# Optimization experiments

Hardware: AMD Instinct MI355X
Metric: run time of the kernel (lower is better)

Reference implementation:

```python
import jax, jax.numpy as jnp
import numpy as np
from jax import lax

B, N, M = 4, 16384, 512
RADIUS2 = 4.0        # radius=2 (hard-coded in forward), compare squared distances
BALL_K = 64          # k=64 hard-coded in forward
KNN_K = 9            # opt.node_knn_k_1
SIGMA_LB = 0.001     # opt.loss_sigma_lower_bound

_DIMS = [("conv1", 6, 64), ("conv2", 64, 64), ("conv3", 64, 64),
         ("conv4", 128, 128), ("conv5", 128, 128),
         ("knnb1", 131, 256), ("knnb2", 256, 256), ("knnb3", 256, 256),
         ("knna1", 512, 512), ("knna2", 512, 512),
         ("mlp1", 640, 512), ("mlp2", 512, 256)]


def setup_inputs() -> dict:
    key = jax.random.key(0)
    ks = jax.random.split(key, 6)
    inp = {
        "x": jax.random.normal(ks[0], (B, 3, N), jnp.float32),
        "sn": jax.random.normal(ks[1], (B, 3, N), jnp.float32),
        "node": jax.random.normal(ks[2], (B, 3, M), jnp.float32),
    }
    for i, (name, cin, cout) in enumerate(_DIMS):
        k = jax.random.fold_in(ks[3], i)
        inp[name + "_w"] = jax.random.normal(k, (cout, cin), jnp.float32) * np.float32(1.0 / np.sqrt(cin))
        inp[name + "_b"] = jnp.zeros((cout,), jnp.float32)
    inp["mlp3_w"] = jax.random.normal(ks[4], (4, 256), jnp.float32) * np.float32(1e-4)  # .normal_(0, 0.0001)
    inp["mlp3_b"] = jnp.zeros((4,), jnp.float32)
    return inp


def _conv(f, w, b, act=True):
    # 1x1 conv over (B,C,M) or (B,C,M,K): channel matmul + bias (+relu)
    y = jnp.einsum('oc,bc...->bo...', w, f) + b.reshape((1, -1) + (1,) * (f.ndim - 2))
    return jax.nn.relu(y) if act else y


def _sqdist(a, b):
    # a: (B,3,Ma), b: (B,3,Nb) -> (B,Ma,Nb) squared euclidean distances
    aa = jnp.sum(a * a, axis=1)
    bb = jnp.sum(b * b, axis=1)
    ab = jnp.einsum('bcm,bcn->bmn', a, b)
    return aa[:, :, None] + bb[:, None, :] - 2.0 * ab


def _gather(feat, idx):
    # feat: (B,C,Nb), idx: (B,Mq,K) -> (B,C,Mq,K)
    Bq, C, _ = feat.shape
    _, Mq, K = idx.shape
    flat = jnp.broadcast_to(idx.reshape(Bq, 1, Mq * K), (Bq, C, Mq * K))
    return jnp.take_along_axis(feat, flat, axis=2).reshape(Bq, C, Mq, K)


def _ball_query(sqd, radius2, k):
    # first k point indices (in original order) with dist<radius, padded by the first hit
    n = sqd.shape[2]
    mask = sqd < radius2
    keyi = jnp.where(mask, jnp.arange(n, dtype=jnp.int32)[None, None, :], jnp.int32(n))
    _, idx = lax.top_k(-keyi, k)  # k smallest keys == first k in-ball indices
    count = jnp.sum(mask, axis=2, keepdims=True)
    return jnp.where(jnp.arange(k)[None, None, :] < count, idx, idx[:, :, :1])


def reference(x, sn, node,
              conv1_w, conv1_b, conv2_w, conv2_b, conv3_w, conv3_b,
              conv4_w, conv4_b, conv5_w, conv5_b,
              knnb1_w, knnb1_b, knnb2_w, knnb2_b, knnb3_w, knnb3_b,
              knna1_w, knna1_b, knna2_w, knna2_b,
              mlp1_w, mlp1_b, mlp2_w, mlp2_b, mlp3_w, mlp3_b):
    x_aug = jnp.concatenate([x, sn], axis=1)                      # (B,6,N)
    idx = _ball_query(_sqdist(node, x), RADIUS2, BALL_K)          # (B,M,64)
    xb = _gather(x_aug, idx)                                      # (B,6,M,64)
    xb = jnp.concatenate([xb[:, :3] - node[:, :, :, None], xb[:, 3:]], axis=1)
    f = _conv(_conv(_conv(xb, conv1_w, conv1_b), conv2_w, conv2_b), conv3_w, conv3_b)
    fmax = jnp.max(f, axis=3, keepdims=True)
    f = jnp.concatenate([f, jnp.broadcast_to(fmax, f.shape)], axis=1)
    f = _conv(_conv(f, conv4_w, conv4_b), conv5_w, conv5_b)
    feat1 = jnp.max(f, axis=3)                                    # (B,128,M)

    # GeneralKNNFusionModule: query=node, database=node, x=feat1, K=KNN_K
    _, knn_idx = lax.top_k(-_sqdist(node, node), KNN_K)           # (B,M,K) nearest nodes
    coords = _gather(node, knn_idx) - node[:, :, :, None]         # (B,3,M,K)
    g = jnp.concatenate([coords, _gather(feat1, knn_idx)], axis=1)  # (B,131,M,K)
    g = _conv(_conv(_conv(g, knnb1_w, knnb1_b), knnb2_w, knnb2_b), knnb3_w, knnb3_b)
    gmax = jnp.max(g, axis=3, keepdims=True)
    g = jnp.concatenate([g, jnp.broadcast_to(gmax, g.shape)], axis=1)
    g = _conv(_conv(g, knna1_w, knna1_b), knna2_w, knna2_b)
    feat2 = jnp.max(g, axis=3)                                    # (B,512,M)

    h = jnp.concatenate([feat1, feat2], axis=1)                   # (B,640,M)
    h = _conv(_conv(h, mlp1_w, mlp1_b), mlp2_w, mlp2_b)
    ksig = _conv(h, mlp3_w, mlp3_b, act=False)                    # (B,4,M)
    keypoints = ksig[:, :3] + node
    sigmas = jax.nn.softplus(ksig[:, 3]) + SIGMA_LB
    return node, keypoints, sigmas
```

## Files before the change

kernel.cpp:

```cpp
#include <hip/hip_runtime.h>

typedef unsigned short u16;
typedef unsigned int u32;
typedef __bf16 bf16x8 __attribute__((ext_vector_type(8)));
typedef float floatx4 __attribute__((ext_vector_type(4)));
typedef unsigned short u16x8 __attribute__((ext_vector_type(8)));
typedef unsigned int u32x4 __attribute__((ext_vector_type(4)));

static constexpr int B_ = 4;
static constexpr int N_ = 16384;
static constexpr int M_ = 512;

__device__ __forceinline__ u16 f2bf(float f) {
    u32 u = __float_as_uint(f);
    u32 r = (u + 0x7fffu + ((u >> 16) & 1u)) >> 16;
    return (u16)r;
}
__device__ __forceinline__ float bf2f(u16 x) {
    return __uint_as_float(((u32)x) << 16);
}
__device__ __forceinline__ u32 pack2(float a, float b) {
    return (u32)f2bf(a) | ((u32)f2bf(b) << 16);
}

__global__ void pack_x_kernel(const float* __restrict__ x, float4* __restrict__ pk) {
    int t = blockIdx.x * 256 + threadIdx.x;
    int b = t >> 14, n = t & (N_ - 1);
    const float* xb = x + (size_t)b * 3 * N_;
    float px = xb[n], py = xb[N_ + n], pz = xb[2 * N_ + n];
    pk[t] = make_float4(px, py, pz, px * px + py * py + pz * pz);
}

__global__ __launch_bounds__(256) void ball_query_kernel(
    const float4* __restrict__ pk, const float* __restrict__ node, int* __restrict__ idx) {
    int bm = blockIdx.x;
    int b = bm >> 9, m = bm & 511;
    int tid = threadIdx.x, wave = tid >> 6, lane = tid & 63;
    __shared__ int sidx[4][64];
    __shared__ int scnt[4];

    const float4* pb = pk + ((size_t)b << 14);
    float nx = node[((size_t)b * 3 + 0) * M_ + m];
    float ny = node[((size_t)b * 3 + 1) * M_ + m];
    float nz = node[((size_t)b * 3 + 2) * M_ + m];
    float aa = nx * nx + ny * ny + nz * nz;

    int cnt = 0;
    int base = wave * 4096;
    for (int n0 = base; n0 < base + 4096; n0 += 64) {
        float4 p = pb[n0 + lane];
        float d = aa + p.w - 2.0f * (nx * p.x + ny * p.y + nz * p.z);
        bool inb = d < 4.0f;
        unsigned long long mask = __ballot(inb);
        if (inb && cnt < 64) {
            int pos = cnt + __popcll(mask & ((1ull << lane) - 1ull));
            if (pos < 64) sidx[wave][pos] = n0 + lane;
        }
        cnt += __popcll(mask);
        if (cnt >= 64) break;
    }
    if (lane == 0) scnt[wave] = cnt;
    __syncthreads();
    if (tid < 64) {
        int total = scnt[0] + scnt[1] + scnt[2] + scnt[3];
        int v = 0;
        if (total > 0) {
            int lim = total < 64 ? total : 64;
            int slot = tid < lim ? tid : 0;
            int w = 0, pre = 0;
            while (w < 3 && slot >= pre + scnt[w]) { pre += scnt[w]; ++w; }
            v = sidx[w][slot - pre];
        }
        idx[(size_t)bm * 64 + tid] = v;
    }
}

__global__ void knn_kernel(const float* __restrict__ node, int* __restrict__ knn) {
    int bm = blockIdx.x;
    int b = bm >> 9, m = bm & 511;
    int lane = threadIdx.x;
    const float* nb = node + (size_t)b * 3 * M_;
    float nx = nb[m], ny = nb[M_ + m], nz = nb[2 * M_ + m];
    float aa = nx * nx + ny * ny + nz * nz;

    float dist[8];
    int didx[8];
#pragma unroll
    for (int i = 0; i < 8; ++i) {
        int n = lane + i * 64;
        float px = nb[n], py = nb[M_ + n], pz = nb[2 * M_ + n];
        float bb = px * px + py * py + pz * pz;
        float ab = nx * px + ny * py + nz * pz;
        dist[i] = aa + bb - 2.0f * ab;
        didx[i] = n;
    }
    for (int r = 0; r < 9; ++r) {
        float bv = dist[0]; int bi = didx[0]; int bslot = 0;
#pragma unroll
        for (int i = 1; i < 8; ++i) {
            if (dist[i] < bv || (dist[i] == bv && didx[i] < bi)) {
                bv = dist[i]; bi = didx[i]; bslot = i;
            }
        }
        float rv = bv; int ri = bi;
        for (int off = 32; off > 0; off >>= 1) {
            float ov = __shfl_down(rv, off);
            int   oi = __shfl_down(ri, off);
            if (ov < rv || (ov == rv && oi < ri)) { rv = ov; ri = oi; }
        }
        ri = __shfl(ri, 0);
        if (lane == 0) knn[(size_t)bm * 9 + r] = ri;
        if (bi == ri) dist[bslot] = 3.0e38f;
    }
}

struct WConvArgs { const float* src[12]; };

__global__ void convert_weights_kernel(WConvArgs args, u16* __restrict__ dst) {
    const int CI[12] = {6, 64, 64, 128, 128, 131, 256, 256, 512, 512, 640, 512};
    const int KP[12] = {32, 64, 64, 128, 128, 160, 256, 256, 512, 512, 640, 512};
    const int OFF[13] = {0, 2048, 6144, 10240, 26624, 43008, 83968, 149504,
                         215040, 477184, 739328, 1067008, 1198080};
    int e = blockIdx.x * 256 + threadIdx.x;
    if (e >= 1198080) return;
    int w = 0;
    while (e >= OFF[w + 1]) ++w;
    int local = e - OFF[w];
    int kp = KP[w];
    int co = local / kp, k = local - co * kp;
    float v = 0.0f;
    if (w == 5) {
        if (k < 3) v = args.src[5][(size_t)co * 131 + k];
        else if (k >= 8 && k < 136) v = args.src[5][(size_t)co * 131 + (k - 5)];
    } else if (k < CI[w]) {
        v = args.src[w][(size_t)co * CI[w] + k];
    }
    dst[e] = f2bf(v);
}

static constexpr int RS = 136;

__device__ __forceinline__ bf16x8 ldsA(const u16* act, int rf, int l15, int quad, int ks) {
    return *(const bf16x8*)(act + (rf * 16 + l15) * RS + ks * 32 + quad * 8);
}
__device__ __forceinline__ bf16x8 ldW(const u16* W, int ks, int l15, int quad, int kstride) {
    return *(const bf16x8*)(W + (size_t)l15 * kstride + ks * 32 + quad * 8);
}

__global__ __launch_bounds__(256) void fused_stage1_kernel(
    const float* __restrict__ x, const float* __restrict__ sn,
    const float* __restrict__ node, const int* __restrict__ idx,
    const u16* __restrict__ Wbf,
    const float* __restrict__ b1, const float* __restrict__ b2,
    const float* __restrict__ b3, const float* __restrict__ b4,
    const float* __restrict__ b5, u16* __restrict__ h) {
    __shared__ __align__(16) u16 act[64 * RS];
    __shared__ __align__(16) u16 mv[64];
    int bm = blockIdx.x;
    int b = bm >> 9, m = bm & 511;
    int tid = threadIdx.x, wave = tid >> 6, lane = tid & 63;
    int quad = lane >> 4, l15 = lane & 15;

    {
        int row = tid & 63, grp = tid >> 6;
        int j = idx[(size_t)bm * 64 + row];
        const float* xb = x + (size_t)b * 3 * N_;
        const float* sb = sn + (size_t)b * 3 * N_;
        if (grp == 0) {
            float c0 = xb[j]      - node[((size_t)b * 3 + 0) * M_ + m];
            float c1 = xb[N_ + j] - node[((size_t)b * 3 + 1) * M_ + m];
            *(u32*)(act + row * RS) = pack2(c0, c1);
        } else if (grp == 1) {
            float c2 = xb[2 * N_ + j] - node[((size_t)b * 3 + 2) * M_ + m];
            *(u32*)(act + row * RS + 2) = pack2(c2, sb[j]);
        } else if (grp == 2) {
            *(u32*)(act + row * RS + 4) = pack2(sb[N_ + j], sb[2 * N_ + j]);
        } else {
            *(u32*)(act + row * RS + 6) = 0u;
            u32x4* r = (u32x4*)(act + row * RS + 8);
            r[0] = (u32x4){0u, 0u, 0u, 0u};
            r[1] = (u32x4){0u, 0u, 0u, 0u};
            r[2] = (u32x4){0u, 0u, 0u, 0u};
        }
    }
    __syncthreads();

    {
        const u16* Wp = Wbf + 0 + (size_t)(wave * 16) * 32;
        bf16x8 bw = ldW(Wp, 0, l15, quad, 32);
        bf16x8 a[4];
#pragma unroll
        for (int rf = 0; rf < 4; ++rf) a[rf] = ldsA(act, rf, l15, quad, 0);
        floatx4 c[4];
#pragma unroll
        for (int rf = 0; rf < 4; ++rf)
            c[rf] = __builtin_amdgcn_mfma_f32_16x16x32_bf16(a[rf], bw, (floatx4){0.f,0.f,0.f,0.f}, 0, 0, 0);
        float bias = b1[wave * 16 + l15];
        __syncthreads();
#pragma unroll
        for (int rf = 0; rf < 4; ++rf)
#pragma unroll
            for (int r = 0; r < 4; ++r)
                act[(rf * 16 + quad * 4 + r) * RS + wave * 16 + l15] = f2bf(fmaxf(c[rf][r] + bias, 0.0f));
        __syncthreads();
    }

    const int WOFF23[2] = {2048, 6144};
    const float* bp23[2] = {b2, b3};
#pragma unroll 1
    for (int cv = 0; cv < 2; ++cv) {
        const u16* Wp = Wbf + WOFF23[cv] + (size_t)(wave * 16) * 64;
        bf16x8 bw[2], a[4][2];
#pragma unroll
        for (int ks = 0; ks < 2; ++ks) bw[ks] = ldW(Wp, ks, l15, quad, 64);
#pragma unroll
        for (int rf = 0; rf < 4; ++rf)
#pragma unroll
            for (int ks = 0; ks < 2; ++ks) a[rf][ks] = ldsA(act, rf, l15, quad, ks);
        floatx4 c[4] = {};
#pragma unroll
        for (int ks = 0; ks < 2; ++ks)
#pragma unroll
            for (int rf = 0; rf < 4; ++rf)
                c[rf] = __builtin_amdgcn_mfma_f32_16x16x32_bf16(a[rf][ks], bw[ks], c[rf], 0, 0, 0);
        float bias = bp23[cv][wave * 16 + l15];
        float v[4][4];
        float mx = 0.0f;
#pragma unroll
        for (int rf = 0; rf < 4; ++rf)
#pragma unroll
            for (int r = 0; r < 4; ++r) {
                v[rf][r] = fmaxf(c[rf][r] + bias, 0.0f);
                mx = fmaxf(mx, v[rf][r]);
            }
        __syncthreads();
#pragma unroll
        for (int rf = 0; rf < 4; ++rf)
#pragma unroll
            for (int r = 0; r < 4; ++r)
                act[(rf * 16 + quad * 4 + r) * RS + wave * 16 + l15] = f2bf(v[rf][r]);
        if (cv == 1) {
            mx = fmaxf(mx, __shfl_xor(mx, 16));
            mx = fmaxf(mx, __shfl_xor(mx, 32));
            if (quad == 0) mv[wave * 16 + l15] = f2bf(mx);
        }
        __syncthreads();
    }

    {
        const u16* Wp = Wbf + 10240 + (size_t)(wave * 32) * 128;
        bf16x8 bw[2][4];
#pragma unroll
        for (int cf = 0; cf < 2; ++cf)
#pragma unroll
            for (int ks = 0; ks < 4; ++ks)
                bw[cf][ks] = ldW(Wp + (size_t)cf * 16 * 128, ks, l15, quad, 128);
        bf16x8 a01[4][2];
#pragma unroll
        for (int rf = 0; rf < 4; ++rf)
#pragma unroll
            for (int ks = 0; ks < 2; ++ks) a01[rf][ks] = ldsA(act, rf, l15, quad, ks);
        bf16x8 am2 = *(const bf16x8*)(mv + quad * 8);
        bf16x8 am3 = *(const bf16x8*)(mv + 32 + quad * 8);
        floatx4 c[4][2] = {};
#pragma unroll
        for (int ks = 0; ks < 4; ++ks) {
#pragma unroll
            for (int rf = 0; rf < 4; ++rf) {
                bf16x8 a = (ks < 2) ? a01[rf][ks] : (ks == 2 ? am2 : am3);
#pragma unroll
                for (int cf = 0; cf < 2; ++cf)
                    c[rf][cf] = __builtin_amdgcn_mfma_f32_16x16x32_bf16(a, bw[cf][ks], c[rf][cf], 0, 0, 0);
            }
        }
        float bias[2];
#pragma unroll
        for (int cf = 0; cf < 2; ++cf) bias[cf] = b4[wave * 32 + cf * 16 + l15];
        __syncthreads();
#pragma unroll
        for (int rf = 0; rf < 4; ++rf)
#pragma unroll
            for (int cf = 0; cf < 2; ++cf)
#pragma unroll
                for (int r = 0; r < 4; ++r)
                    act[(rf * 16 + quad * 4 + r) * RS + wave * 32 + cf * 16 + l15] =
                        f2bf(fmaxf(c[rf][cf][r] + bias[cf], 0.0f));
        __syncthreads();
    }

    {
        const u16* Wp = Wbf + 26624 + (size_t)(wave * 32) * 128;
        bf16x8 bw[2][4];
#pragma unroll
        for (int cf = 0; cf < 2; ++cf)
#pragma unroll
            for (int ks = 0; ks < 4; ++ks)
                bw[cf][ks] = ldW(Wp + (size_t)cf * 16 * 128, ks, l15, quad, 128);
        floatx4 c[4][2] = {};
#pragma unroll
        for (int ks = 0; ks < 4; ++ks) {
#pragma unroll
            for (int rf = 0; rf < 4; ++rf) {
                bf16x8 a = ldsA(act, rf, l15, quad, ks);
#pragma unroll
                for (int cf = 0; cf < 2; ++cf)
                    c[rf][cf] = __builtin_amdgcn_mfma_f32_16x16x32_bf16(a, bw[cf][ks], c[rf][cf], 0, 0, 0);
            }
        }
#pragma unroll
        for (int cf = 0; cf < 2; ++cf) {
            float bias = b5[wave * 32 + cf * 16 + l15];
            float mx = 0.0f;
#pragma unroll
            for (int rf = 0; rf < 4; ++rf)
#pragma unroll
                for (int r = 0; r < 4; ++r)
                    mx = fmaxf(mx, fmaxf(c[rf][cf][r] + bias, 0.0f));
            mx = fmaxf(mx, __shfl_xor(mx, 16));
            mx = fmaxf(mx, __shfl_xor(mx, 32));
            if (quad == 0) h[(size_t)bm * 640 + wave * 32 + cf * 16 + l15] = f2bf(mx);
        }
    }
}

template <int KS, int CF, int RF, int RSx>
__device__ __forceinline__ void conv_inplace(u16* act, const u16* __restrict__ W0, int KP,
                                             const float* __restrict__ bias, int cb,
                                             int l15, int quad) {
    floatx4 acc[RF][CF];
#pragma unroll
    for (int rf = 0; rf < RF; ++rf)
#pragma unroll
        for (int cf = 0; cf < CF; ++cf) acc[rf][cf] = (floatx4){0.f, 0.f, 0.f, 0.f};

    bf16x8 bwA[CF], bwB[CF];
#pragma unroll
    for (int cf = 0; cf < CF; ++cf)
        bwA[cf] = *(const bf16x8*)(W0 + (size_t)(cb + cf * 16 + l15) * KP + quad * 8);

#pragma unroll
    for (int ks = 0; ks < KS; ++ks) {
        bf16x8* cur = (ks % 2 == 0) ? bwA : bwB;
        bf16x8* nxt = (ks % 2 == 0) ? bwB : bwA;
        if (ks + 1 < KS) {
#pragma unroll
            for (int cf = 0; cf < CF; ++cf)
                nxt[cf] = *(const bf16x8*)(W0 + (size_t)(cb + cf * 16 + l15) * KP +
                                           (ks + 1) * 32 + quad * 8);
        }
#pragma unroll
        for (int rf = 0; rf < RF; ++rf) {
            bf16x8 a = *(const bf16x8*)(act + (rf * 16 + l15) * RSx + ks * 32 + quad * 8);
#pragma unroll
            for (int cf = 0; cf < CF; ++cf)
                acc[rf][cf] = __builtin_amdgcn_mfma_f32_16x16x32_bf16(a, cur[cf], acc[rf][cf], 0, 0, 0);
        }
    }
    __syncthreads();
#pragma unroll
    for (int cf = 0; cf < CF; ++cf) {
        float bs = bias[cb + cf * 16 + l15];
#pragma unroll
        for (int rf = 0; rf < RF; ++rf)
#pragma unroll
            for (int r = 0; r < 4; ++r)
                act[(rf * 16 + quad * 4 + r) * RSx + cb + cf * 16 + l15] =
                    f2bf(fmaxf(acc[rf][cf][r] + bs, 0.0f));
    }
    __syncthreads();
}

static constexpr int RS2 = 520;

__global__ __launch_bounds__(512, 1) void fused_stage2_kernel(
    const float* __restrict__ node, u16* __restrict__ h, const int* __restrict__ knn,
    const u16* __restrict__ Wbf,
    const float* __restrict__ bb1, const float* __restrict__ bb2,
    const float* __restrict__ bb3, const float* __restrict__ ba1,
    const float* __restrict__ ba2) {
    __shared__ __align__(16) u16 act[80 * RS2];
    int blk = blockIdx.x;
    int node0 = blk * 8;
    int b = node0 >> 9;
    int tid = threadIdx.x, wave = tid >> 6, lane = tid & 63;
    int quad = lane >> 4, l15 = lane & 15;
    (void)lane;

    for (int e = tid; e < 80 * 20; e += 512)
        *(u16x8*)(act + (e / 20) * RS2 + (e % 20) * 8) = (u16x8){0,0,0,0,0,0,0,0};
    __syncthreads();
    for (int e = tid; e < 72 * 3; e += 512) {
        int r = e / 3, c = e - r * 3;
        int nodei = node0 + r / 9;
        int j = knn[(size_t)nodei * 9 + (r % 9)];
        float v = node[((size_t)b * 3 + c) * M_ + j] - node[((size_t)b * 3 + c) * M_ + (nodei & 511)];
        act[r * RS2 + c] = f2bf(v);
    }
    for (int e = tid; e < 72 * 16; e += 512) {
        int r = e >> 4, s = e & 15;
        int nodei = node0 + r / 9;
        int j = knn[(size_t)nodei * 9 + (r % 9)];
        *(u16x8*)(act + r * RS2 + 8 + s * 8) =
            *(const u16x8*)(h + (size_t)(b * 512 + j) * 640 + s * 8);
    }
    __syncthreads();

    conv_inplace<5, 2, 5, RS2>(act, Wbf + 43008, 160, bb1, wave * 32, l15, quad);
    conv_inplace<8, 2, 5, RS2>(act, Wbf + 83968, 256, bb2, wave * 32, l15, quad);
    conv_inplace<8, 2, 5, RS2>(act, Wbf + 149504, 256, bb3, wave * 32, l15, quad);

    for (int e = tid; e < 8 * 32; e += 512) {
        int li = e >> 5, s = e & 31;
        int r0 = li * 9;
        float mx[8];
#pragma unroll
        for (int i = 0; i < 8; ++i) mx[i] = -3.0e38f;
#pragma unroll
        for (int kk = 0; kk < 9; ++kk) {
            u16x8 v = *(const u16x8*)(act + (r0 + kk) * RS2 + s * 8);
#pragma unroll
            for (int i = 0; i < 8; ++i) mx[i] = fmaxf(mx[i], bf2f(v[i]));
        }
        u16x8 o;
#pragma unroll
        for (int i = 0; i < 8; ++i) o[i] = f2bf(mx[i]);
#pragma unroll
        for (int kk = 0; kk < 9; ++kk)
            *(u16x8*)(act + (r0 + kk) * RS2 + 256 + s * 8) = o;
    }
    __syncthreads();

    conv_inplace<16, 4, 5, RS2>(act, Wbf + 215040, 512, ba1, wave * 64, l15, quad);
    conv_inplace<16, 4, 5, RS2>(act, Wbf + 477184, 512, ba2, wave * 64, l15, quad);

    for (int e = tid; e < 8 * 64; e += 512) {
        int li = e >> 6, s = e & 63;
        int r0 = li * 9;
        float mx[8];
#pragma unroll
        for (int i = 0; i < 8; ++i) mx[i] = -3.0e38f;
#pragma unroll
        for (int kk = 0; kk < 9; ++kk) {
            u16x8 v = *(const u16x8*)(act + (r0 + kk) * RS2 + s * 8);
#pragma unroll
            for (int i = 0; i < 8; ++i) mx[i] = fmaxf(mx[i], bf2f(v[i]));
        }
        u16x8 o;
#pragma unroll
        for (int i = 0; i < 8; ++i) o[i] = f2bf(mx[i]);
        *(u16x8*)(h + (size_t)(node0 + li) * 640 + 128 + s * 8) = o;
    }
}

static constexpr int RS3 = 648;

__global__ __launch_bounds__(512, 1) void fused_stage3_kernel(
    const float* __restrict__ node, const u16* __restrict__ h,
    const u16* __restrict__ Wbf,
    const float* __restrict__ bm1, const float* __restrict__ bm2,
    const float* __restrict__ w3, const float* __restrict__ b3,
    float* __restrict__ out) {
    __shared__ __align__(16) u16 act[16 * RS3];
    int blk = blockIdx.x;
    int node0 = blk * 16;
    int tid = threadIdx.x, lane = tid & 63, wave = tid >> 6;
    int quad = lane >> 4, l15 = lane & 15;

    for (int e = tid; e < 16 * 80; e += 512) {
        int r = e / 80, seg = e - r * 80;
        *(u16x8*)(act + r * RS3 + seg * 8) = *(const u16x8*)(h + (size_t)(node0 + r) * 640 + seg * 8);
    }
    __syncthreads();

    conv_inplace<20, 4, 1, RS3>(act, Wbf + 739328, 640, bm1, wave * 64, l15, quad);
    conv_inplace<16, 2, 1, RS3>(act, Wbf + 1067008, 512, bm2, wave * 32, l15, quad);

    if (tid < 64) {
        int li = tid >> 2, oc = tid & 3;
        const u16* row = act + li * RS3;
        const float* wrow = w3 + oc * 256;
        float a = 0.0f;
        for (int c = 0; c < 256; c += 4) {
            a += bf2f(row[c]) * wrow[c];
            a += bf2f(row[c + 1]) * wrow[c + 1];
            a += bf2f(row[c + 2]) * wrow[c + 2];
            a += bf2f(row[c + 3]) * wrow[c + 3];
        }
        a += b3[oc];
        int nodei = node0 + li;
        int b = nodei >> 9, m = nodei & 511;
        if (oc < 3) {
            float nv = node[((size_t)b * 3 + oc) * M_ + m];
            out[((size_t)b * 3 + oc) * M_ + m] = nv;
            out[6144 + ((size_t)b * 3 + oc) * M_ + m] = nv + a;
        } else {
            out[12288 + nodei] = fmaxf(a, 0.0f) + log1pf(expf(-fabsf(a))) + 0.001f;
        }
    }
}

extern "C" void kernel_launch(void* const* d_in, const int* in_sizes, int n_in,
                              void* d_out, int out_size, void* d_ws, size_t ws_size,
                              hipStream_t stream) {
    (void)in_sizes; (void)n_in; (void)out_size; (void)ws_size;
    const float* x = (const float*)d_in[0];
    const float* sn = (const float*)d_in[1];
    const float* node = (const float*)d_in[2];
    const float* W[13];
    const float* Bs[13];
    for (int i = 0; i < 13; ++i) {
        W[i] = (const float*)d_in[3 + 2 * i];
        Bs[i] = (const float*)d_in[4 + 2 * i];
    }
    float* out = (float*)d_out;

    char* ws = (char*)d_ws;
    int* idx = (int*)(ws + 0);
    int* knn = (int*)(ws + 524288);
    u16* Wbf = (u16*)(ws + 598016);
    u16* h   = (u16*)(ws + 2994176);
    float4* pk = (float4*)(ws + 5615616);

    WConvArgs wa;
    for (int w = 0; w < 12; ++w) wa.src[w] = W[w];
    convert_weights_kernel<<<(1198080 + 255) / 256, 256, 0, stream>>>(wa, Wbf);

    pack_x_kernel<<<256, 256, 0, stream>>>(x, pk);
    ball_query_kernel<<<2048, 256, 0, stream>>>(pk, node, idx);
    knn_kernel<<<2048, 64, 0, stream>>>(node, knn);

    fused_stage1_kernel<<<2048, 256, 0, stream>>>(x, sn, node, idx, Wbf,
                                                  Bs[0], Bs[1], Bs[2], Bs[3], Bs[4], h);
    fused_stage2_kernel<<<256, 512, 0, stream>>>(node, h, knn, Wbf,
                                                 Bs[5], Bs[6], Bs[7], Bs[8], Bs[9]);
    fused_stage3_kernel<<<128, 512, 0, stream>>>(node, h, Wbf, Bs[10], Bs[11],
                                                 W[12], Bs[12], out);
}
```

Measured before the change: 262.1 us.

## Rebalance work split across fused stage kernels: two nodes per stage1 block, wider stage2, smaller stage3

Stage1 now processes two ball-query groups per block (128 rows), so each loaded weight fragment is reused across twice as many MFMA tiles and half as many blocks are launched. Stage2 doubles its block to 1024 threads, with each wave owning half as many output channels. Stage3 handles 8 nodes per block with zero-padded rows, doubling the grid to 256 blocks for better CU coverage at the cost of wasted MFMA work on padded rows. Higher register pressure in stage1 and the larger stage2 blocks may reduce occupancy.

```diff
diff --git a/kernel.cpp b/kernel.cpp
--- a/kernel.cpp
+++ b/kernel.cpp
@@ -147,58 +147,58 @@
     return *(const bf16x8*)(W + (size_t)l15 * kstride + ks * 32 + quad * 8);
 }
 
-__global__ __launch_bounds__(256) void fused_stage1_kernel(
+__global__ __launch_bounds__(256, 2) void fused_stage1_kernel(
     const float* __restrict__ x, const float* __restrict__ sn,
     const float* __restrict__ node, const int* __restrict__ idx,
     const u16* __restrict__ Wbf,
     const float* __restrict__ b1, const float* __restrict__ b2,
     const float* __restrict__ b3, const float* __restrict__ b4,
     const float* __restrict__ b5, u16* __restrict__ h) {
-    __shared__ __align__(16) u16 act[64 * RS];
-    __shared__ __align__(16) u16 mv[64];
-    int bm = blockIdx.x;
-    int b = bm >> 9, m = bm & 511;
+    __shared__ __align__(16) u16 act[128 * RS];
+    __shared__ __align__(16) u16 mv[2][64];
+    int blk = blockIdx.x;
+    int bm0 = blk * 2;
     int tid = threadIdx.x, wave = tid >> 6, lane = tid & 63;
     int quad = lane >> 4, l15 = lane & 15;
 
     {
-        int row = tid & 63, grp = tid >> 6;
-        int j = idx[(size_t)bm * 64 + row];
+        int row = tid & 127, grp = tid >> 7;
+        int bm = bm0 + (row >> 6);
+        int b = bm >> 9, m = bm & 511;
+        int j = idx[(size_t)bm * 64 + (row & 63)];
         const float* xb = x + (size_t)b * 3 * N_;
         const float* sb = sn + (size_t)b * 3 * N_;
+        u16* r = act + row * RS;
         if (grp == 0) {
-            float c0 = xb[j]      - node[((size_t)b * 3 + 0) * M_ + m];
-            float c1 = xb[N_ + j] - node[((size_t)b * 3 + 1) * M_ + m];
-            *(u32*)(act + row * RS) = pack2(c0, c1);
-        } else if (grp == 1) {
+            float c0 = xb[j]          - node[((size_t)b * 3 + 0) * M_ + m];
+            float c1 = xb[N_ + j]     - node[((size_t)b * 3 + 1) * M_ + m];
             float c2 = xb[2 * N_ + j] - node[((size_t)b * 3 + 2) * M_ + m];
-            *(u32*)(act + row * RS + 2) = pack2(c2, sb[j]);
-        } else if (grp == 2) {
-            *(u32*)(act + row * RS + 4) = pack2(sb[N_ + j], sb[2 * N_ + j]);
+            *(u32*)(r)     = pack2(c0, c1);
+            *(u32*)(r + 2) = pack2(c2, sb[j]);
         } else {
-            *(u32*)(act + row * RS + 6) = 0u;
-            u32x4* r = (u32x4*)(act + row * RS + 8);
-            r[0] = (u32x4){0u, 0u, 0u, 0u};
-            r[1] = (u32x4){0u, 0u, 0u, 0u};
-            r[2] = (u32x4){0u, 0u, 0u, 0u};
+            *(u32*)(r + 4) = pack2(sb[N_ + j], sb[2 * N_ + j]);
+            *(u32*)(r + 6) = 0u;
+            u32x4* z = (u32x4*)(r + 8);
+            z[0] = (u32x4){0u, 0u, 0u, 0u};
+            z[1] = (u32x4){0u, 0u, 0u, 0u};
+            z[2] = (u32x4){0u, 0u, 0u, 0u};
         }
     }
     __syncthreads();
 
     {
-        const u16* Wp = Wbf + 0 + (size_t)(wave * 16) * 32;
+        const u16* Wp = Wbf + (size_t)(wave * 16) * 32;
         bf16x8 bw = ldW(Wp, 0, l15, quad, 32);
-        bf16x8 a[4];
-#pragma unroll
-        for (int rf = 0; rf < 4; ++rf) a[rf] = ldsA(act, rf, l15, quad, 0);
-        floatx4 c[4];
-#pragma unroll
-        for (int rf = 0; rf < 4; ++rf)
-            c[rf] = __builtin_amdgcn_mfma_f32_16x16x32_bf16(a[rf], bw, (floatx4){0.f,0.f,0.f,0.f}, 0, 0, 0);
+        floatx4 c[8];
+#pragma unroll
+        for (int rf = 0; rf < 8; ++rf) {
+            bf16x8 a = ldsA(act, rf, l15, quad, 0);
+            c[rf] = __builtin_amdgcn_mfma_f32_16x16x32_bf16(a, bw, (floatx4){0.f,0.f,0.f,0.f}, 0, 0, 0);
+        }
         float bias = b1[wave * 16 + l15];
         __syncthreads();
 #pragma unroll
-        for (int rf = 0; rf < 4; ++rf)
+        for (int rf = 0; rf < 8; ++rf)
 #pragma unroll
             for (int r = 0; r < 4; ++r)
                 act[(rf * 16 + quad * 4 + r) * RS + wave * 16 + l15] = f2bf(fmaxf(c[rf][r] + bias, 0.0f));
@@ -210,39 +210,40 @@
 #pragma unroll 1
     for (int cv = 0; cv < 2; ++cv) {
         const u16* Wp = Wbf + WOFF23[cv] + (size_t)(wave * 16) * 64;
-        bf16x8 bw[2], a[4][2];
-#pragma unroll
-        for (int ks = 0; ks < 2; ++ks) bw[ks] = ldW(Wp, ks, l15, quad, 64);
-#pragma unroll
-        for (int rf = 0; rf < 4; ++rf)
-#pragma unroll
-            for (int ks = 0; ks < 2; ++ks) a[rf][ks] = ldsA(act, rf, l15, quad, ks);
-        floatx4 c[4] = {};
+        bf16x8 bw0 = ldW(Wp, 0, l15, quad, 64);
+        bf16x8 bw1 = ldW(Wp, 1, l15, quad, 64);
+        floatx4 c[8] = {};
 #pragma unroll
         for (int ks = 0; ks < 2; ++ks)
 #pragma unroll
-            for (int rf = 0; rf < 4; ++rf)
-                c[rf] = __builtin_amdgcn_mfma_f32_16x16x32_bf16(a[rf][ks], bw[ks], c[rf], 0, 0, 0);
+            for (int rf = 0; rf < 8; ++rf) {
+                bf16x8 a = ldsA(act, rf, l15, quad, ks);
+                c[rf] = __builtin_amdgcn_mfma_f32_16x16x32_bf16(a, ks ? bw1 : bw0, c[rf], 0, 0, 0);
+            }
         float bias = bp23[cv][wave * 16 + l15];
-        float v[4][4];
-        float mx = 0.0f;
-#pragma unroll
-        for (int rf = 0; rf < 4; ++rf)
+        float mxA = 0.0f, mxB = 0.0f;
+#pragma unroll
+        for (int rf = 0; rf < 8; ++rf)
 #pragma unroll
             for (int r = 0; r < 4; ++r) {
-                v[rf][r] = fmaxf(c[rf][r] + bias, 0.0f);
-                mx = fmaxf(mx, v[rf][r]);
+                float v = fmaxf(c[rf][r] + bias, 0.0f);
+                if (rf < 4) mxA = fmaxf(mxA, v); else mxB = fmaxf(mxB, v);
             }
         __syncthreads();
 #pragma unroll
-        for (int rf = 0; rf < 4; ++rf)
+        for (int rf = 0; rf < 8; ++rf)
 #pragma unroll
             for (int r = 0; r < 4; ++r)
-                act[(rf * 16 + quad * 4 + r) * RS + wave * 16 + l15] = f2bf(v[rf][r]);
+                act[(rf * 16 + quad * 4 + r) * RS + wave * 16 + l15] = f2bf(fmaxf(c[rf][r] + bias, 0.0f));
         if (cv == 1) {
-            mx = fmaxf(mx, __shfl_xor(mx, 16));
-            mx = fmaxf(mx, __shfl_xor(mx, 32));
-            if (quad == 0) mv[wave * 16 + l15] = f2bf(mx);
+            mxA = fmaxf(mxA, __shfl_xor(mxA, 16));
+            mxA = fmaxf(mxA, __shfl_xor(mxA, 32));
+            mxB = fmaxf(mxB, __shfl_xor(mxB, 16));
+            mxB = fmaxf(mxB, __shfl_xor(mxB, 32));
+            if (quad == 0) {
+                mv[0][wave * 16 + l15] = f2bf(mxA);
+                mv[1][wave * 16 + l15] = f2bf(mxB);
+            }
         }
         __syncthreads();
     }
@@ -255,30 +256,23 @@
 #pragma unroll
             for (int ks = 0; ks < 4; ++ks)
                 bw[cf][ks] = ldW(Wp + (size_t)cf * 16 * 128, ks, l15, quad, 128);
-        bf16x8 a01[4][2];
-#pragma unroll
-        for (int rf = 0; rf < 4; ++rf)
-#pragma unroll
-            for (int ks = 0; ks < 2; ++ks) a01[rf][ks] = ldsA(act, rf, l15, quad, ks);
-        bf16x8 am2 = *(const bf16x8*)(mv + quad * 8);
-        bf16x8 am3 = *(const bf16x8*)(mv + 32 + quad * 8);
-        floatx4 c[4][2] = {};
-#pragma unroll
-        for (int ks = 0; ks < 4; ++ks) {
-#pragma unroll
-            for (int rf = 0; rf < 4; ++rf) {
-                bf16x8 a = (ks < 2) ? a01[rf][ks] : (ks == 2 ? am2 : am3);
+        floatx4 c[8][2] = {};
+#pragma unroll
+        for (int ks = 0; ks < 4; ++ks)
+#pragma unroll
+            for (int rf = 0; rf < 8; ++rf) {
+                bf16x8 a = (ks < 2) ? ldsA(act, rf, l15, quad, ks)
+                                    : *(const bf16x8*)(&mv[rf >> 2][(ks - 2) * 32 + quad * 8]);
 #pragma unroll
                 for (int cf = 0; cf < 2; ++cf)
                     c[rf][cf] = __builtin_amdgcn_mfma_f32_16x16x32_bf16(a, bw[cf][ks], c[rf][cf], 0, 0, 0);
             }
-        }
         float bias[2];
 #pragma unroll
         for (int cf = 0; cf < 2; ++cf) bias[cf] = b4[wave * 32 + cf * 16 + l15];
         __syncthreads();
 #pragma unroll
-        for (int rf = 0; rf < 4; ++rf)
+        for (int rf = 0; rf < 8; ++rf)
 #pragma unroll
             for (int cf = 0; cf < 2; ++cf)
 #pragma unroll
@@ -296,29 +290,35 @@
 #pragma unroll
             for (int ks = 0; ks < 4; ++ks)
                 bw[cf][ks] = ldW(Wp + (size_t)cf * 16 * 128, ks, l15, quad, 128);
-        floatx4 c[4][2] = {};
-#pragma unroll
-        for (int ks = 0; ks < 4; ++ks) {
-#pragma unroll
-            for (int rf = 0; rf < 4; ++rf) {
+        floatx4 c[8][2] = {};
+#pragma unroll
+        for (int ks = 0; ks < 4; ++ks)
+#pragma unroll
+            for (int rf = 0; rf < 8; ++rf) {
                 bf16x8 a = ldsA(act, rf, l15, quad, ks);
 #pragma unroll
                 for (int cf = 0; cf < 2; ++cf)
                     c[rf][cf] = __builtin_amdgcn_mfma_f32_16x16x32_bf16(a, bw[cf][ks], c[rf][cf], 0, 0, 0);
             }
-        }
 #pragma unroll
         for (int cf = 0; cf < 2; ++cf) {
             float bias = b5[wave * 32 + cf * 16 + l15];
-            float mx = 0.0f;
-#pragma unroll
-            for (int rf = 0; rf < 4; ++rf)
-#pragma unroll
-                for (int r = 0; r < 4; ++r)
-                    mx = fmaxf(mx, fmaxf(c[rf][cf][r] + bias, 0.0f));
-            mx = fmaxf(mx, __shfl_xor(mx, 16));
-            mx = fmaxf(mx, __shfl_xor(mx, 32));
-            if (quad == 0) h[(size_t)bm * 640 + wave * 32 + cf * 16 + l15] = f2bf(mx);
+            float mxA = 0.0f, mxB = 0.0f;
+#pragma unroll
+            for (int rf = 0; rf < 8; ++rf)
+#pragma unroll
+                for (int r = 0; r < 4; ++r) {
+                    float v = fmaxf(c[rf][cf][r] + bias, 0.0f);
+                    if (rf < 4) mxA = fmaxf(mxA, v); else mxB = fmaxf(mxB, v);
+                }
+            mxA = fmaxf(mxA, __shfl_xor(mxA, 16));
+            mxA = fmaxf(mxA, __shfl_xor(mxA, 32));
+            mxB = fmaxf(mxB, __shfl_xor(mxB, 16));
+            mxB = fmaxf(mxB, __shfl_xor(mxB, 32));
+            if (quad == 0) {
+                h[(size_t)bm0 * 640 + wave * 32 + cf * 16 + l15] = f2bf(mxA);
+                h[(size_t)(bm0 + 1) * 640 + wave * 32 + cf * 16 + l15] = f2bf(mxB);
+            }
         }
     }
 }
@@ -372,7 +372,7 @@
 
 static constexpr int RS2 = 520;
 
-__global__ __launch_bounds__(512, 1) void fused_stage2_kernel(
+__global__ __launch_bounds__(1024, 4) void fused_stage2_kernel(
     const float* __restrict__ node, u16* __restrict__ h, const int* __restrict__ knn,
     const u16* __restrict__ Wbf,
     const float* __restrict__ bb1, const float* __restrict__ bb2,
@@ -386,17 +386,17 @@
     int quad = lane >> 4, l15 = lane & 15;
     (void)lane;
 
-    for (int e = tid; e < 80 * 20; e += 512)
+    for (int e = tid; e < 80 * 20; e += 1024)
         *(u16x8*)(act + (e / 20) * RS2 + (e % 20) * 8) = (u16x8){0,0,0,0,0,0,0,0};
     __syncthreads();
-    for (int e = tid; e < 72 * 3; e += 512) {
+    for (int e = tid; e < 72 * 3; e += 1024) {
         int r = e / 3, c = e - r * 3;
         int nodei = node0 + r / 9;
         int j = knn[(size_t)nodei * 9 + (r % 9)];
         float v = node[((size_t)b * 3 + c) * M_ + j] - node[((size_t)b * 3 + c) * M_ + (nodei & 511)];
         act[r * RS2 + c] = f2bf(v);
     }
-    for (int e = tid; e < 72 * 16; e += 512) {
+    for (int e = tid; e < 72 * 16; e += 1024) {
         int r = e >> 4, s = e & 15;
         int nodei = node0 + r / 9;
         int j = knn[(size_t)nodei * 9 + (r % 9)];
@@ -405,11 +405,11 @@
     }
     __syncthreads();
 
-    conv_inplace<5, 2, 5, RS2>(act, Wbf + 43008, 160, bb1, wave * 32, l15, quad);
-    conv_inplace<8, 2, 5, RS2>(act, Wbf + 83968, 256, bb2, wave * 32, l15, quad);
-    conv_inplace<8, 2, 5, RS2>(act, Wbf + 149504, 256, bb3, wave * 32, l15, quad);
-
-    for (int e = tid; e < 8 * 32; e += 512) {
+    conv_inplace<5, 1, 5, RS2>(act, Wbf + 43008, 160, bb1, wave * 16, l15, quad);
+    conv_inplace<8, 1, 5, RS2>(act, Wbf + 83968, 256, bb2, wave * 16, l15, quad);
+    conv_inplace<8, 1, 5, RS2>(act, Wbf + 149504, 256, bb3, wave * 16, l15, quad);
+
+    for (int e = tid; e < 8 * 32; e += 1024) {
         int li = e >> 5, s = e & 31;
         int r0 = li * 9;
         float mx[8];
@@ -430,10 +430,10 @@
     }
     __syncthreads();
 
-    conv_inplace<16, 4, 5, RS2>(act, Wbf + 215040, 512, ba1, wave * 64, l15, quad);
-    conv_inplace<16, 4, 5, RS2>(act, Wbf + 477184, 512, ba2, wave * 64, l15, quad);
-
-    for (int e = tid; e < 8 * 64; e += 512) {
+    conv_inplace<16, 2, 5, RS2>(act, Wbf + 215040, 512, ba1, wave * 32, l15, quad);
+    conv_inplace<16, 2, 5, RS2>(act, Wbf + 477184, 512, ba2, wave * 32, l15, quad);
+
+    for (int e = tid; e < 8 * 64; e += 1024) {
         int li = e >> 6, s = e & 63;
         int r0 = li * 9;
         float mx[8];
@@ -454,7 +454,7 @@
 
 static constexpr int RS3 = 648;
 
-__global__ __launch_bounds__(512, 1) void fused_stage3_kernel(
+__global__ __launch_bounds__(512, 2) void fused_stage3_kernel(
     const float* __restrict__ node, const u16* __restrict__ h,
     const u16* __restrict__ Wbf,
     const float* __restrict__ bm1, const float* __restrict__ bm2,
@@ -462,20 +462,22 @@
     float* __restrict__ out) {
     __shared__ __align__(16) u16 act[16 * RS3];
     int blk = blockIdx.x;
-    int node0 = blk * 16;
+    int node0 = blk * 8;
     int tid = threadIdx.x, lane = tid & 63, wave = tid >> 6;
     int quad = lane >> 4, l15 = lane & 15;
 
     for (int e = tid; e < 16 * 80; e += 512) {
         int r = e / 80, seg = e - r * 80;
-        *(u16x8*)(act + r * RS3 + seg * 8) = *(const u16x8*)(h + (size_t)(node0 + r) * 640 + seg * 8);
+        u16x8 v = (r < 8) ? *(const u16x8*)(h + (size_t)(node0 + r) * 640 + seg * 8)
+                          : (u16x8){0,0,0,0,0,0,0,0};
+        *(u16x8*)(act + r * RS3 + seg * 8) = v;
     }
     __syncthreads();
 
     conv_inplace<20, 4, 1, RS3>(act, Wbf + 739328, 640, bm1, wave * 64, l15, quad);
     conv_inplace<16, 2, 1, RS3>(act, Wbf + 1067008, 512, bm2, wave * 32, l15, quad);
 
-    if (tid < 64) {
+    if (tid < 32) {
         int li = tid >> 2, oc = tid & 3;
         const u16* row = act + li * RS3;
         const float* wrow = w3 + oc * 256;
@@ -529,10 +531,10 @@
     ball_query_kernel<<<2048, 256, 0, stream>>>(pk, node, idx);
     knn_kernel<<<2048, 64, 0, stream>>>(node, knn);
 
-    fused_stage1_kernel<<<2048, 256, 0, stream>>>(x, sn, node, idx, Wbf,
+    fused_stage1_kernel<<<1024, 256, 0, stream>>>(x, sn, node, idx, Wbf,
                                                   Bs[0], Bs[1], Bs[2], Bs[3], Bs[4], h);
-    fused_stage2_kernel<<<256, 512, 0, stream>>>(node, h, knn, Wbf,
-                                                 Bs[5], Bs[6], Bs[7], Bs[8], Bs[9]);
-    fused_stage3_kernel<<<128, 512, 0, stream>>>(node, h, Wbf, Bs[10], Bs[11],
+    fused_stage2_kernel<<<256, 1024, 0, stream>>>(node, h, knn, Wbf,
+                                                  Bs[5], Bs[6], Bs[7], Bs[8], Bs[9]);
+    fused_stage3_kernel<<<256, 512, 0, stream>>>(node, h, Wbf, Bs[10], Bs[11],
                                                  W[12], Bs[12], out);
 }
```

Result: no change. 257.6 us (-1.7%).
